# Optimization experiments

Hardware: AMD Instinct MI355X
Metric: run time of the kernel (lower is better)

## Reference

```python
import jax, jax.numpy as jnp
import numpy as np

D = 512
H = 8
LQ = 2048
LK = 8192
LARGE_NEG = 10000.0
CLAMP = 20.0


def setup_inputs() -> dict:
    key = jax.random.key(0)
    ks = jax.random.split(key, 9)
    Q = jax.random.normal(ks[0], (LQ, D), dtype=jnp.float32)
    K = jax.random.normal(ks[1], (LK, D), dtype=jnp.float32)
    V = jax.random.normal(ks[2], (LK, D), dtype=jnp.float32)
    key_padding_mask = jax.random.randint(ks[3], (LK,), 0, 2).astype(jnp.bool_)
    per_query_key_bias = jax.random.normal(ks[4], (LQ, LK), dtype=jnp.float32)
    # learned params of nn.MultiheadAttention: packed in_proj + out_proj
    s = 1.0 / np.sqrt(D)
    W_in = jax.random.uniform(ks[5], (3 * D, D), jnp.float32, -s, s)
    b_in = jnp.zeros((3 * D,), jnp.float32)
    W_out = jax.random.uniform(ks[6], (D, D), jnp.float32, -s, s)
    b_out = jnp.zeros((D,), jnp.float32)
    return {"Q": Q, "K": K, "V": V, "key_padding_mask": key_padding_mask,
            "per_query_key_bias": per_query_key_bias,
            "W_in": W_in, "b_in": b_in, "W_out": W_out, "b_out": b_out}


def reference(Q, K, V, key_padding_mask, per_query_key_bias, W_in, b_in, W_out, b_out):
    d = D // H
    # packed QKV projections (F.linear: x @ W.T + b)
    q = Q @ W_in[:D].T + b_in[:D]            # [Lq, D]
    k = K @ W_in[D:2 * D].T + b_in[D:2 * D]  # [Lk, D]
    v = V @ W_in[2 * D:].T + b_in[2 * D:]    # [Lk, D]
    q = q.reshape(LQ, H, d)
    k = k.reshape(LK, H, d)
    v = v.reshape(LK, H, d)
    scale = 1.0 / jnp.sqrt(jnp.asarray(d, q.dtype))
    scores = jnp.einsum('qhd,khd->hqk', q, k) * scale  # [H, Lq, Lk]
    scores = scores + per_query_key_bias[None, :, :]
    # column-only padding mask with large negative (no -inf)
    pad = key_padding_mask.astype(scores.dtype)[None, None, :]
    scores = scores - LARGE_NEG * pad
    # amax stabilization then clamp, then softmax
    scores = scores - jnp.max(scores, axis=-1, keepdims=True)
    scores = jnp.clip(scores, -CLAMP, CLAMP)
    attn = jax.nn.softmax(scores, axis=-1)
    out = jnp.einsum('hqk,khd->qhd', attn, v).reshape(LQ, D)
    out = out @ W_out.T + b_out
    return out
```

## Files before the change

### kernel.cpp

```cpp
#include <hip/hip_runtime.h>
#include <math.h>

#define DD 512
#define NH 8
#define HD 64
#define NLQ 2048
#define NLK 8192
#define LOG2E 1.4426950408889634f
#define SCQ (0.125f * LOG2E)

typedef __attribute__((ext_vector_type(8))) short bf16x8;
typedef __attribute__((ext_vector_type(8))) unsigned short u16x8;
typedef __attribute__((ext_vector_type(4))) float f32x4;

#define MFMA16(a, b, c) __builtin_amdgcn_mfma_f32_16x16x32_bf16((a), (b), (c), 0, 0, 0)

__device__ __forceinline__ unsigned short f2bf(float x) {
    unsigned u = __builtin_bit_cast(unsigned, x);
    u += 0x7fffu + ((u >> 16) & 1u);
    return (unsigned short)(u >> 16);
}
__device__ __forceinline__ float bf2f(unsigned short h) {
    unsigned u = ((unsigned)h) << 16;
    return __builtin_bit_cast(float, u);
}
__device__ __forceinline__ unsigned short f2h(float x) {
    return __builtin_bit_cast(unsigned short, (_Float16)x);
}
__device__ __forceinline__ float h2f(unsigned short u) {
    return (float)__builtin_bit_cast(_Float16, u);
}
__device__ __forceinline__ int cvtpk(float a, float b) {
    int r;
    asm("v_cvt_pk_bf16_f32 %0, %1, %2" : "=v"(r) : "v"(a), "v"(b));
    return r;
}
__device__ __forceinline__ float max3f(float a, float b, float c) {
    return fmaxf(fmaxf(a, b), c);
}
__device__ __forceinline__ float lobf(int w) {
    return __builtin_bit_cast(float, w << 16);
}
__device__ __forceinline__ float hibf(int w) {
    return __builtin_bit_cast(float, (int)(w & 0xffff0000));
}

#define NPROJ 576

__global__ __launch_bounds__(256) void prep(const float* __restrict__ Q,
                                            const float* __restrict__ K,
                                            const float* __restrict__ V,
                                            const float* __restrict__ Win,
                                            const float* __restrict__ bin,
                                            const float* __restrict__ bias,
                                            const int* __restrict__ mask,
                                            short* __restrict__ qhi,
                                            short* __restrict__ khi,
                                            short* __restrict__ vthi,
                                            unsigned short* __restrict__ bh)
{
    __shared__ __align__(16) short XsH[128 * 40];
    __shared__ __align__(16) short WsH[128 * 40];
    __shared__ __align__(16) short WsL[128 * 40];

    const int bid = blockIdx.x;
    if (bid >= NPROJ) {
        const int tid  = (bid - NPROJ) * 256 + threadIdx.x;
        const int tile = tid >> 6;
        const int l    = tid & 63;
        const int q    = (tile >> 7) * 16 + (l & 15);
        const int kb   = (tile & 127) * 64 + 4 * (l >> 4);
        u16x8 o0v, o1v;
#pragma unroll
        for (int j = 0; j < 4; ++j) {
            const float4 bv = *(const float4*)&bias[(size_t)q * NLK + kb + 16 * j];
            const int4   mv = *(const int4*)&mask[kb + 16 * j];
            const float a[4] = {bv.x, bv.y, bv.z, bv.w};
            const int   m[4] = {mv.x, mv.y, mv.z, mv.w};
#pragma unroll
            for (int r = 0; r < 4; ++r) {
                const float v = (a[r] - 10000.f * (float)m[r]) * LOG2E;
                const int idx = j * 4 + r;
                if (idx < 8) o0v[idx] = f2h(v);
                else         o1v[idx - 8] = f2h(v);
            }
        }
        const size_t base = ((size_t)tid) * 16;
        *(u16x8*)&bh[base] = o0v;
        *(u16x8*)&bh[base + 8] = o1v;
        return;
    }

    const int o0 = (bid / 144) * 128;
    const int bx = bid % 144;
    const float* X; const float* Wf; const float* b; short* out;
    int r0; float scale; int tr;
    if (bx < 16)      { X = Q; r0 = bx * 128;        Wf = Win;               b = bin;          out = qhi;  scale = SCQ; tr = 0; }
    else if (bx < 80) { X = K; r0 = (bx - 16) * 128; Wf = Win + DD * DD;     b = bin + DD;     out = khi;  scale = 1.f; tr = 0; }
    else              { X = V; r0 = (bx - 80) * 128; Wf = Win + 2 * DD * DD; b = bin + 2 * DD; out = vthi; scale = 1.f; tr = 1; }

    const int t    = threadIdx.x;
    const int wid  = t >> 6;
    const int lane = t & 63;
    const int g  = lane >> 4;
    const int c  = lane & 15;
    const int wr = wid >> 1;
    const int wc = wid & 1;
    const int srow = t >> 1;
    const int sk   = (t & 1) * 16;

    float4 xf[4], wf[4];
    auto ld = [&](int kc) {
#pragma unroll
        for (int i = 0; i < 4; ++i) {
            xf[i] = *(const float4*)&X[(size_t)(r0 + srow) * DD + kc + sk + 4 * i];
            wf[i] = *(const float4*)&Wf[(size_t)(o0 + srow) * DD + kc + sk + 4 * i];
        }
    };
    auto st = [&]() {
#pragma unroll
        for (int i = 0; i < 2; ++i) {
            int4 xw;
            xw.x = cvtpk(xf[2 * i].x, xf[2 * i].y);
            xw.y = cvtpk(xf[2 * i].z, xf[2 * i].w);
            xw.z = cvtpk(xf[2 * i + 1].x, xf[2 * i + 1].y);
            xw.w = cvtpk(xf[2 * i + 1].z, xf[2 * i + 1].w);
            *(int4*)&XsH[srow * 40 + sk + 8 * i] = xw;
            const float4 a = wf[2 * i], bb = wf[2 * i + 1];
            int4 hw;
            hw.x = cvtpk(a.x, a.y);
            hw.y = cvtpk(a.z, a.w);
            hw.z = cvtpk(bb.x, bb.y);
            hw.w = cvtpk(bb.z, bb.w);
            int4 lw;
            lw.x = cvtpk(a.x - lobf(hw.x), a.y - hibf(hw.x));
            lw.y = cvtpk(a.z - lobf(hw.y), a.w - hibf(hw.y));
            lw.z = cvtpk(bb.x - lobf(hw.z), bb.y - hibf(hw.z));
            lw.w = cvtpk(bb.z - lobf(hw.w), bb.w - hibf(hw.w));
            *(int4*)&WsH[srow * 40 + sk + 8 * i] = hw;
            *(int4*)&WsL[srow * 40 + sk + 8 * i] = lw;
        }
    };

    f32x4 acc[4][4];
#pragma unroll
    for (int i = 0; i < 4; ++i)
#pragma unroll
        for (int j = 0; j < 4; ++j) acc[i][j] = (f32x4){0.f, 0.f, 0.f, 0.f};

    ld(0);
    for (int kc = 0; kc < DD; kc += 32) {
        __syncthreads();
        st();
        __syncthreads();
        if (kc + 32 < DD) ld(kc + 32);

        bf16x8 ah[4], bhf[4], blf[4];
#pragma unroll
        for (int qg = 0; qg < 4; ++qg)
            ah[qg] = *(const bf16x8*)&XsH[(64 * wr + 16 * qg + c) * 40 + 8 * g];
#pragma unroll
        for (int og = 0; og < 4; ++og) {
            const int adr = (64 * wc + 16 * og + c) * 40 + 8 * g;
            bhf[og] = *(const bf16x8*)&WsH[adr];
            blf[og] = *(const bf16x8*)&WsL[adr];
        }
#pragma unroll
        for (int qg = 0; qg < 4; ++qg)
#pragma unroll
            for (int og = 0; og < 4; ++og) {
                acc[qg][og] = MFMA16(ah[qg], bhf[og], acc[qg][og]);
                acc[qg][og] = MFMA16(ah[qg], blf[og], acc[qg][og]);
            }
    }

#pragma unroll
    for (int qg = 0; qg < 4; ++qg)
#pragma unroll
        for (int og = 0; og < 4; ++og) {
            const int col = o0 + 64 * wc + 16 * og + c;
            const float bo = b[col];
#pragma unroll
            for (int r = 0; r < 4; ++r) {
                const int row = r0 + 64 * wr + 16 * qg + 4 * g + r;
                const float v = (acc[qg][og][r] + bo) * scale;
                if (tr) out[(size_t)col * NLK + row] = (short)f2bf(v);
                else    out[(size_t)row * DD + col]  = (short)f2bf(v);
            }
        }
}

__global__ __launch_bounds__(256) void gemm_out(const short* __restrict__ Xhi,
                                                const short* __restrict__ Xlo,
                                                const float* __restrict__ Wf,
                                                const float* __restrict__ b,
                                                float* __restrict__ Y)
{
    __shared__ __align__(16) short XsH[64 * 40];
    __shared__ __align__(16) short XsL[64 * 40];
    __shared__ __align__(16) short WsH[64 * 40];
    __shared__ __align__(16) short WsL[64 * 40];

    const int r0 = blockIdx.x * 64;
    const int o0 = blockIdx.y * 64;
    const int t    = threadIdx.x;
    const int wid  = t >> 6;
    const int lane = t & 63;
    const int g  = lane >> 4;
    const int c  = lane & 15;
    const int srow = t >> 2;
    const int sc8  = (t & 3) * 8;

    bf16x8 pxh, pxl;
    float4 wf0, wf1;
    auto ld = [&](int kc) {
        pxh = *(const bf16x8*)&Xhi[(size_t)(r0 + srow) * DD + kc + sc8];
        pxl = *(const bf16x8*)&Xlo[(size_t)(r0 + srow) * DD + kc + sc8];
        wf0 = *(const float4*)&Wf[(size_t)(o0 + srow) * DD + kc + sc8];
        wf1 = *(const float4*)&Wf[(size_t)(o0 + srow) * DD + kc + sc8 + 4];
    };
    auto st = [&]() {
        *(bf16x8*)&XsH[srow * 40 + sc8] = pxh;
        *(bf16x8*)&XsL[srow * 40 + sc8] = pxl;
        int4 hw;
        hw.x = cvtpk(wf0.x, wf0.y);
        hw.y = cvtpk(wf0.z, wf0.w);
        hw.z = cvtpk(wf1.x, wf1.y);
        hw.w = cvtpk(wf1.z, wf1.w);
        int4 lw;
        lw.x = cvtpk(wf0.x - lobf(hw.x), wf0.y - hibf(hw.x));
        lw.y = cvtpk(wf0.z - lobf(hw.y), wf0.w - hibf(hw.y));
        lw.z = cvtpk(wf1.x - lobf(hw.z), wf1.y - hibf(hw.z));
        lw.w = cvtpk(wf1.z - lobf(hw.w), wf1.w - hibf(hw.w));
        *(int4*)&WsH[srow * 40 + sc8] = hw;
        *(int4*)&WsL[srow * 40 + sc8] = lw;
    };

    f32x4 acc[4];
#pragma unroll
    for (int n = 0; n < 4; ++n) acc[n] = (f32x4){0.f, 0.f, 0.f, 0.f};

    ld(0);
    for (int kc = 0; kc < DD; kc += 32) {
        __syncthreads();
        st();
        __syncthreads();
        if (kc + 32 < DD) ld(kc + 32);

        bf16x8 ah, al, bh[4], bl[4];
        ah = *(const bf16x8*)&XsH[(wid * 16 + c) * 40 + 8 * g];
        al = *(const bf16x8*)&XsL[(wid * 16 + c) * 40 + 8 * g];
#pragma unroll
        for (int n = 0; n < 4; ++n) {
            const int adr = (16 * n + c) * 40 + 8 * g;
            bh[n] = *(const bf16x8*)&WsH[adr];
            bl[n] = *(const bf16x8*)&WsL[adr];
        }
#pragma unroll
        for (int n = 0; n < 4; ++n) {
            acc[n] = MFMA16(ah, bh[n], acc[n]);
            acc[n] = MFMA16(ah, bl[n], acc[n]);
            acc[n] = MFMA16(al, bh[n], acc[n]);
        }
    }

#pragma unroll
    for (int n = 0; n < 4; ++n) {
        const int col = o0 + 16 * n + c;
        const float bo = b[col];
#pragma unroll
        for (int r = 0; r < 4; ++r)
            Y[(size_t)(r0 + wid * 16 + 4 * g + r) * DD + col] = acc[n][r] + bo;
    }
}

#define QT 128
#define KT 64
#define NKC 8
#define CHUNK (NLK / NKC)
#define NT (CHUNK / KT)

__global__ __launch_bounds__(512, 4) void attn_mfma(const short* __restrict__ qhi,
                                                    const short* __restrict__ khi,
                                                    const short* __restrict__ vthi,
                                                    const unsigned short* __restrict__ biash,
                                                    unsigned short* __restrict__ macc,
                                                    float2* __restrict__ mlb)
{
    __shared__ __align__(16) short ksh[2 * KT * HD];
    __shared__ __align__(16) short vth[2 * KT * HD];
    __shared__ __align__(16) short psh[8 * 16 * KT];

    const int id = blockIdx.x;
    const int h  = id >> 7;
    const int qt = (id >> 3) & 15;
    const int kc = id & 7;
    const int q0 = qt * QT;
    const int k0 = kc * CHUNK;

    const int t    = threadIdx.x;
    const int wid  = t >> 6;
    const int lane = t & 63;
    const int g  = lane >> 4;
    const int cl = lane & 15;
    const int swc = ((cl & 7) << 3);

    bf16x8 qah[2];
    {
        const size_t qr = (size_t)(q0 + wid * 16 + cl) * DD + h * HD;
        qah[0] = *(const bf16x8*)&qhi[qr + 8 * g];
        qah[1] = *(const bf16x8*)&qhi[qr + 32 + 8 * g];
    }

    const int v0 = (8 * g) ^ swc;
    const short* kbA0 = &ksh[cl * HD + v0];
    const short* kbB0 = &ksh[cl * HD + (v0 ^ 32)];
    const short* kbA1 = kbA0 + KT * HD;
    const short* kbB1 = kbB0 + KT * HD;
    const short* vbA0 = &vth[cl * HD + v0];
    const short* vbB0 = &vth[cl * HD + (v0 ^ 32)];
    const short* vbA1 = vbA0 + KT * HD;
    const short* vbB1 = vbB0 + KT * HD;

    const int kr0 = t >> 3;
    const int db0 = (t & 7) * 8;
    const int sw0 = ((kr0 & 7) << 3);
    short* wk0 = &ksh[kr0 * HD + (db0 ^ sw0)];
    short* wk1 = wk0 + KT * HD;
    short* wv0 = &vth[kr0 * HD + (db0 ^ sw0)];
    short* wv1 = wv0 + KT * HD;

    short* psw = &psh[wid * (16 * KT)];
    short* pw0 = &psw[cl * KT + (( 0 + 4 * g) ^ swc)];
    short* pw1 = &psw[cl * KT + ((16 + 4 * g) ^ swc)];
    short* pw2 = &psw[cl * KT + ((32 + 4 * g) ^ swc)];
    short* pw3 = &psw[cl * KT + ((48 + 4 * g) ^ swc)];
    const short* pr0 = &psw[cl * KT + ((8 * g) ^ swc)];
    const short* pr1 = &psw[cl * KT + ((32 + 8 * g) ^ swc)];

    const short* kgp = khi + (size_t)(k0 + kr0) * DD + h * HD + db0;
    const short* vgp = vthi + (size_t)(h * HD + kr0) * NLK + k0 + db0;
    const unsigned short* bgp =
        biash + (((size_t)(qt * 8 + wid) * 128 + kc * NT) << 10) + lane * 16;

    bf16x8 rkh, rvh;
    u16x8 bp0, bp1;
    rkh = *(const bf16x8*)kgp;  kgp += (size_t)KT * DD;
    rvh = *(const bf16x8*)vgp;  vgp += KT;
    bp0 = *(const u16x8*)bgp;
    bp1 = *(const u16x8*)(bgp + 8);  bgp += 1024;

    bf16x8 ones;
#pragma unroll
    for (int i = 0; i < 8; ++i) ones[i] = (short)0x3F80;

    f32x4 acco[4];
    f32x4 lacc = (f32x4){0.f, 0.f, 0.f, 0.f};
#pragma unroll
    for (int n = 0; n < 4; ++n) acco[n] = (f32x4){0.f, 0.f, 0.f, 0.f};
    float m_ = -1e30f;

    for (int it = 0; it < NT; ++it) {
        const int p = it & 1;
        const short* kA = p ? kbA1 : kbA0;
        const short* kB = p ? kbB1 : kbB0;
        const short* vA = p ? vbA1 : vbA0;
        const short* vB = p ? vbB1 : vbB0;
        short* wk = p ? wk1 : wk0;
        short* wv = p ? wv1 : wv0;

        *(bf16x8*)wk = rkh;
        *(bf16x8*)wv = rvh;
        __syncthreads();
        if (it + 1 < NT) {
            rkh = *(const bf16x8*)kgp;  kgp += (size_t)KT * DD;
            rvh = *(const bf16x8*)vgp;  vgp += KT;
        }

        f32x4 sc[4];
#pragma unroll
        for (int j = 0; j < 4; ++j)
#pragma unroll
            for (int r = 0; r < 4; ++r) {
                const int i = j * 4 + r;
                sc[j][r] = h2f((i < 8) ? (unsigned short)bp0[i]
                                       : (unsigned short)bp1[i - 8]);
            }

        __builtin_amdgcn_s_setprio(1);
#pragma unroll
        for (int j = 0; j < 4; ++j) {
            const bf16x8 kf0 = *(const bf16x8*)(kA + j * 16 * HD);
            const bf16x8 kf1 = *(const bf16x8*)(kB + j * 16 * HD);
            sc[j] = MFMA16(kf0, qah[0], sc[j]);
            sc[j] = MFMA16(kf1, qah[1], sc[j]);
        }
        __builtin_amdgcn_s_setprio(0);

        if (it + 1 < NT) {
            bp0 = *(const u16x8*)bgp;
            bp1 = *(const u16x8*)(bgp + 8);  bgp += 1024;
        }

        const float t0 = max3f(sc[0][0], sc[0][1], sc[0][2]);
        const float t1 = max3f(sc[0][3], sc[1][0], sc[1][1]);
        const float t2 = max3f(sc[1][2], sc[1][3], sc[2][0]);
        const float t3 = max3f(sc[2][1], sc[2][2], sc[2][3]);
        const float t4 = max3f(sc[3][0], sc[3][1], sc[3][2]);
        float tm = max3f(max3f(t0, t1, t2), max3f(t3, t4, sc[3][3]),
                         -1e30f);
        tm = fmaxf(tm, __shfl_xor(tm, 16));
        tm = fmaxf(tm, __shfl_xor(tm, 32));
        if (!__all(tm - m_ <= 11.5f)) {
            const float mn = fmaxf(m_, tm);
            const float al = exp2f(m_ - mn);
            float alr[4];
#pragma unroll
            for (int r = 0; r < 4; ++r) alr[r] = __shfl(al, 4 * g + r);
#pragma unroll
            for (int n = 0; n < 4; ++n)
#pragma unroll
                for (int r = 0; r < 4; ++r) acco[n][r] *= alr[r];
#pragma unroll
            for (int r = 0; r < 4; ++r) lacc[r] *= alr[r];
            m_ = mn;
        }
#pragma unroll
        for (int j = 0; j < 4; ++j)
#pragma unroll
            for (int r = 0; r < 4; ++r)
                sc[j][r] = exp2f(sc[j][r] - m_);

        *(int2*)pw0 = make_int2(cvtpk(sc[0][0], sc[0][1]), cvtpk(sc[0][2], sc[0][3]));
        *(int2*)pw1 = make_int2(cvtpk(sc[1][0], sc[1][1]), cvtpk(sc[1][2], sc[1][3]));
        *(int2*)pw2 = make_int2(cvtpk(sc[2][0], sc[2][1]), cvtpk(sc[2][2], sc[2][3]));
        *(int2*)pw3 = make_int2(cvtpk(sc[3][0], sc[3][1]), cvtpk(sc[3][2], sc[3][3]));
        bf16x8 pah[2];
        pah[0] = *(const bf16x8*)pr0;
        pah[1] = *(const bf16x8*)pr1;

        __builtin_amdgcn_s_setprio(1);
#pragma unroll
        for (int n = 0; n < 4; ++n) {
            const bf16x8 vh0 = *(const bf16x8*)(vA + n * 16 * HD);
            const bf16x8 vh1 = *(const bf16x8*)(vB + n * 16 * HD);
            acco[n] = MFMA16(pah[0], vh0, acco[n]);
            acco[n] = MFMA16(pah[1], vh1, acco[n]);
        }
        lacc = MFMA16(pah[0], ones, lacc);
        lacc = MFMA16(pah[1], ones, lacc);
        __builtin_amdgcn_s_setprio(0);
    }

    f32x4 linv;
#pragma unroll
    for (int r = 0; r < 4; ++r) linv[r] = 1.f / lacc[r];
#pragma unroll
    for (int r = 0; r < 4; ++r) {
        const int q = q0 + wid * 16 + 4 * g + r;
        const size_t base = ((size_t)(kc * NH + h) * NLQ + q) * HD;
#pragma unroll
        for (int n = 0; n < 4; ++n)
            macc[base + 16 * n + cl] = f2h(acco[n][r] * linv[r]);
    }
    {
        const int srcl = ((cl >> 2) << 4) + cl;
        const float lc0 = __shfl(lacc[0], srcl);
        const float lc1 = __shfl(lacc[1], srcl);
        const float lc2 = __shfl(lacc[2], srcl);
        const float lc3 = __shfl(lacc[3], srcl);
        const int rr = cl & 3;
        const float lq = rr == 0 ? lc0 : rr == 1 ? lc1 : rr == 2 ? lc2 : lc3;
        if (g == 0)
            mlb[(size_t)(kc * NH + h) * NLQ + q0 + wid * 16 + cl] = make_float2(m_, lq);
    }
}

__global__ __launch_bounds__(256) void attn_combine(const unsigned short* __restrict__ macc,
                                                    const float2* __restrict__ mlb,
                                                    short* __restrict__ aohi,
                                                    short* __restrict__ aolo)
{
    const int row = blockIdx.x * 4 + (threadIdx.x >> 6);
    const int d   = threadIdx.x & 63;
    float m[NKC], l[NKC];
#pragma unroll
    for (int c = 0; c < NKC; ++c) {
        const float2 v = mlb[(size_t)c * NH * NLQ + row];
        m[c] = v.x; l[c] = v.y;
    }
    float M = m[0];
#pragma unroll
    for (int c = 1; c < NKC; ++c) M = fmaxf(M, m[c]);
    float w[NKC], L = 0.f;
#pragma unroll
    for (int c = 0; c < NKC; ++c) { w[c] = exp2f(m[c] - M) * l[c]; L += w[c]; }
    float s = 0.f;
#pragma unroll
    for (int c = 0; c < NKC; ++c)
        s += h2f(macc[((size_t)c * NH * NLQ + row) * HD + d]) * w[c];
    const float v = s / L;
    const int hh = row >> 11;
    const int q  = row & (NLQ - 1);
    const size_t o = (size_t)q * DD + hh * HD + d;
    const unsigned short hb = f2bf(v);
    aohi[o] = (short)hb;
    aolo[o] = (short)f2bf(v - bf2f(hb));
}

extern "C" void kernel_launch(void* const* d_in, const int* in_sizes, int n_in,
                              void* d_out, int out_size, void* d_ws, size_t ws_size,
                              hipStream_t stream)
{
    (void)in_sizes; (void)n_in; (void)out_size; (void)ws_size;
    const float* Q    = (const float*)d_in[0];
    const float* K    = (const float*)d_in[1];
    const float* V    = (const float*)d_in[2];
    const int*   mask = (const int*)d_in[3];
    const float* bias = (const float*)d_in[4];
    const float* Win  = (const float*)d_in[5];
    const float* bin  = (const float*)d_in[6];
    const float* Wout = (const float*)d_in[7];
    const float* bout = (const float*)d_in[8];
    float* out = (float*)d_out;

    short* qhi_  = (short*)d_ws;
    short* khi_  = qhi_  + (size_t)NLQ * DD;
    short* vthi_ = khi_  + (size_t)NLK * DD;
    unsigned short* biash_ = (unsigned short*)(vthi_ + (size_t)NLK * DD);
    unsigned short* macc_  = biash_ + (size_t)NLQ * NLK;
    float2* ml_  = (float2*)(macc_ + (size_t)NKC * NH * NLQ * HD);
    short* aohi_ = (short*)(ml_ + (size_t)NKC * NH * NLQ);
    short* aolo_ = aohi_ + (size_t)NLQ * DD;

    prep<<<dim3(NPROJ + 4096), 256, 0, stream>>>(Q, K, V, Win, bin, bias, mask,
                                                 qhi_, khi_, vthi_, biash_);

    attn_mfma<<<dim3(NH * 16 * NKC), 512, 0, stream>>>(qhi_, khi_, vthi_, biash_, macc_, ml_);

    attn_combine<<<dim3(NH * NLQ / 4), 256, 0, stream>>>(macc_, ml_, aohi_, aolo_);

    gemm_out<<<dim3(NLQ / 64, DD / 64), 256, 0, stream>>>(aohi_, aolo_, Wout, bout, out);
}
```

Baseline: 145.1 us.

## Process two 16-row query subtiles per wave to double K/V reuse

```diff
diff --git a/kernel.cpp b/kernel.cpp
--- a/kernel.cpp
+++ b/kernel.cpp
@@ -274,11 +274,12 @@
     }
 }
 
-#define QT 128
+#define QT 256
 #define KT 64
 #define NKC 8
 #define CHUNK (NLK / NKC)
 #define NT (CHUNK / KT)
+#define BOFF (128 * 1024)
 
 __global__ __launch_bounds__(512, 4) void attn_mfma(const short* __restrict__ qhi,
                                                     const short* __restrict__ khi,
@@ -292,8 +293,8 @@
     __shared__ __align__(16) short psh[8 * 16 * KT];
 
     const int id = blockIdx.x;
-    const int h  = id >> 7;
-    const int qt = (id >> 3) & 15;
+    const int h  = id >> 6;
+    const int qt = (id >> 3) & 7;
     const int kc = id & 7;
     const int q0 = qt * QT;
     const int k0 = kc * CHUNK;
@@ -305,11 +306,13 @@
     const int cl = lane & 15;
     const int swc = ((cl & 7) << 3);
 
-    bf16x8 qah[2];
+    bf16x8 qaA[2], qaB[2];
     {
-        const size_t qr = (size_t)(q0 + wid * 16 + cl) * DD + h * HD;
-        qah[0] = *(const bf16x8*)&qhi[qr + 8 * g];
-        qah[1] = *(const bf16x8*)&qhi[qr + 32 + 8 * g];
+        const size_t qrA = (size_t)(q0 + wid * 32 + cl) * DD + h * HD;
+        qaA[0] = *(const bf16x8*)&qhi[qrA + 8 * g];
+        qaA[1] = *(const bf16x8*)&qhi[qrA + 32 + 8 * g];
+        qaB[0] = *(const bf16x8*)&qhi[qrA + 16 * DD + 8 * g];
+        qaB[1] = *(const bf16x8*)&qhi[qrA + 16 * DD + 32 + 8 * g];
     }
 
     const int v0 = (8 * g) ^ swc;
@@ -341,24 +344,68 @@
     const short* kgp = khi + (size_t)(k0 + kr0) * DD + h * HD + db0;
     const short* vgp = vthi + (size_t)(h * HD + kr0) * NLK + k0 + db0;
     const unsigned short* bgp =
-        biash + (((size_t)(qt * 8 + wid) * 128 + kc * NT) << 10) + lane * 16;
+        biash + (((size_t)(qt * 16 + wid * 2) * 128 + kc * NT) << 10) + lane * 16;
 
     bf16x8 rkh, rvh;
-    u16x8 bp0, bp1;
+    u16x8 bpA0, bpA1, bpB0, bpB1;
     rkh = *(const bf16x8*)kgp;  kgp += (size_t)KT * DD;
     rvh = *(const bf16x8*)vgp;  vgp += KT;
-    bp0 = *(const u16x8*)bgp;
-    bp1 = *(const u16x8*)(bgp + 8);  bgp += 1024;
+    bpA0 = *(const u16x8*)bgp;
+    bpA1 = *(const u16x8*)(bgp + 8);
+    bpB0 = *(const u16x8*)(bgp + BOFF);
+    bpB1 = *(const u16x8*)(bgp + BOFF + 8);
+    bgp += 1024;
 
     bf16x8 ones;
 #pragma unroll
     for (int i = 0; i < 8; ++i) ones[i] = (short)0x3F80;
 
-    f32x4 acco[4];
-    f32x4 lacc = (f32x4){0.f, 0.f, 0.f, 0.f};
-#pragma unroll
-    for (int n = 0; n < 4; ++n) acco[n] = (f32x4){0.f, 0.f, 0.f, 0.f};
-    float m_ = -1e30f;
+    f32x4 accA[4], accB[4];
+    f32x4 lacA = (f32x4){0.f, 0.f, 0.f, 0.f};
+    f32x4 lacB = (f32x4){0.f, 0.f, 0.f, 0.f};
+#pragma unroll
+    for (int n = 0; n < 4; ++n) {
+        accA[n] = (f32x4){0.f, 0.f, 0.f, 0.f};
+        accB[n] = (f32x4){0.f, 0.f, 0.f, 0.f};
+    }
+    float mA = -1e30f, mB = -1e30f;
+
+    auto softmax_pack = [&](f32x4 (&sc)[4], f32x4 (&acc)[4], f32x4 &lac,
+                            float &mm, bf16x8 (&pa)[2]) {
+        const float t0 = max3f(sc[0][0], sc[0][1], sc[0][2]);
+        const float t1 = max3f(sc[0][3], sc[1][0], sc[1][1]);
+        const float t2 = max3f(sc[1][2], sc[1][3], sc[2][0]);
+        const float t3 = max3f(sc[2][1], sc[2][2], sc[2][3]);
+        const float t4 = max3f(sc[3][0], sc[3][1], sc[3][2]);
+        float tm = max3f(max3f(t0, t1, t2), max3f(t3, t4, sc[3][3]), -1e30f);
+        tm = fmaxf(tm, __shfl_xor(tm, 16));
+        tm = fmaxf(tm, __shfl_xor(tm, 32));
+        if (!__all(tm - mm <= 11.5f)) {
+            const float mn = fmaxf(mm, tm);
+            const float al = exp2f(mm - mn);
+            float alr[4];
+#pragma unroll
+            for (int r = 0; r < 4; ++r) alr[r] = __shfl(al, 4 * g + r);
+#pragma unroll
+            for (int n = 0; n < 4; ++n)
+#pragma unroll
+                for (int r = 0; r < 4; ++r) acc[n][r] *= alr[r];
+#pragma unroll
+            for (int r = 0; r < 4; ++r) lac[r] *= alr[r];
+            mm = mn;
+        }
+#pragma unroll
+        for (int j = 0; j < 4; ++j)
+#pragma unroll
+            for (int r = 0; r < 4; ++r)
+                sc[j][r] = exp2f(sc[j][r] - mm);
+        *(int2*)pw0 = make_int2(cvtpk(sc[0][0], sc[0][1]), cvtpk(sc[0][2], sc[0][3]));
+        *(int2*)pw1 = make_int2(cvtpk(sc[1][0], sc[1][1]), cvtpk(sc[1][2], sc[1][3]));
+        *(int2*)pw2 = make_int2(cvtpk(sc[2][0], sc[2][1]), cvtpk(sc[2][2], sc[2][3]));
+        *(int2*)pw3 = make_int2(cvtpk(sc[3][0], sc[3][1]), cvtpk(sc[3][2], sc[3][3]));
+        pa[0] = *(const bf16x8*)pr0;
+        pa[1] = *(const bf16x8*)pr1;
+    };
 
     for (int it = 0; it < NT; ++it) {
         const int p = it & 1;
@@ -377,14 +424,16 @@
             rvh = *(const bf16x8*)vgp;  vgp += KT;
         }
 
-        f32x4 sc[4];
+        f32x4 scA[4], scB[4];
 #pragma unroll
         for (int j = 0; j < 4; ++j)
 #pragma unroll
             for (int r = 0; r < 4; ++r) {
                 const int i = j * 4 + r;
-                sc[j][r] = h2f((i < 8) ? (unsigned short)bp0[i]
-                                       : (unsigned short)bp1[i - 8]);
+                scA[j][r] = h2f((i < 8) ? (unsigned short)bpA0[i]
+                                        : (unsigned short)bpA1[i - 8]);
+                scB[j][r] = h2f((i < 8) ? (unsigned short)bpB0[i]
+                                        : (unsigned short)bpB1[i - 8]);
             }
 
         __builtin_amdgcn_s_setprio(1);
@@ -392,88 +441,66 @@
         for (int j = 0; j < 4; ++j) {
             const bf16x8 kf0 = *(const bf16x8*)(kA + j * 16 * HD);
             const bf16x8 kf1 = *(const bf16x8*)(kB + j * 16 * HD);
-            sc[j] = MFMA16(kf0, qah[0], sc[j]);
-            sc[j] = MFMA16(kf1, qah[1], sc[j]);
+            scA[j] = MFMA16(kf0, qaA[0], scA[j]);
+            scA[j] = MFMA16(kf1, qaA[1], scA[j]);
+            scB[j] = MFMA16(kf0, qaB[0], scB[j]);
+            scB[j] = MFMA16(kf1, qaB[1], scB[j]);
         }
         __builtin_amdgcn_s_setprio(0);
 
-        if (it + 1 < NT) {
-            bp0 = *(const u16x8*)bgp;
-            bp1 = *(const u16x8*)(bgp + 8);  bgp += 1024;
-        }
-
-        const float t0 = max3f(sc[0][0], sc[0][1], sc[0][2]);
-        const float t1 = max3f(sc[0][3], sc[1][0], sc[1][1]);
-        const float t2 = max3f(sc[1][2], sc[1][3], sc[2][0]);
-        const float t3 = max3f(sc[2][1], sc[2][2], sc[2][3]);
-        const float t4 = max3f(sc[3][0], sc[3][1], sc[3][2]);
-        float tm = max3f(max3f(t0, t1, t2), max3f(t3, t4, sc[3][3]),
-                         -1e30f);
-        tm = fmaxf(tm, __shfl_xor(tm, 16));
-        tm = fmaxf(tm, __shfl_xor(tm, 32));
-        if (!__all(tm - m_ <= 11.5f)) {
-            const float mn = fmaxf(m_, tm);
-            const float al = exp2f(m_ - mn);
-            float alr[4];
-#pragma unroll
-            for (int r = 0; r < 4; ++r) alr[r] = __shfl(al, 4 * g + r);
-#pragma unroll
-            for (int n = 0; n < 4; ++n)
-#pragma unroll
-                for (int r = 0; r < 4; ++r) acco[n][r] *= alr[r];
-#pragma unroll
-            for (int r = 0; r < 4; ++r) lacc[r] *= alr[r];
-            m_ = mn;
-        }
-#pragma unroll
-        for (int j = 0; j < 4; ++j)
-#pragma unroll
-            for (int r = 0; r < 4; ++r)
-                sc[j][r] = exp2f(sc[j][r] - m_);
-
-        *(int2*)pw0 = make_int2(cvtpk(sc[0][0], sc[0][1]), cvtpk(sc[0][2], sc[0][3]));
-        *(int2*)pw1 = make_int2(cvtpk(sc[1][0], sc[1][1]), cvtpk(sc[1][2], sc[1][3]));
-        *(int2*)pw2 = make_int2(cvtpk(sc[2][0], sc[2][1]), cvtpk(sc[2][2], sc[2][3]));
-        *(int2*)pw3 = make_int2(cvtpk(sc[3][0], sc[3][1]), cvtpk(sc[3][2], sc[3][3]));
-        bf16x8 pah[2];
-        pah[0] = *(const bf16x8*)pr0;
-        pah[1] = *(const bf16x8*)pr1;
+        bf16x8 paA[2], paB[2];
+        softmax_pack(scA, accA, lacA, mA, paA);
+        softmax_pack(scB, accB, lacB, mB, paB);
 
         __builtin_amdgcn_s_setprio(1);
 #pragma unroll
         for (int n = 0; n < 4; ++n) {
             const bf16x8 vh0 = *(const bf16x8*)(vA + n * 16 * HD);
             const bf16x8 vh1 = *(const bf16x8*)(vB + n * 16 * HD);
-            acco[n] = MFMA16(pah[0], vh0, acco[n]);
-            acco[n] = MFMA16(pah[1], vh1, acco[n]);
-        }
-        lacc = MFMA16(pah[0], ones, lacc);
-        lacc = MFMA16(pah[1], ones, lacc);
+            accA[n] = MFMA16(paA[0], vh0, accA[n]);
+            accA[n] = MFMA16(paA[1], vh1, accA[n]);
+            accB[n] = MFMA16(paB[0], vh0, accB[n]);
+            accB[n] = MFMA16(paB[1], vh1, accB[n]);
+        }
+        lacA = MFMA16(paA[0], ones, lacA);
+        lacA = MFMA16(paA[1], ones, lacA);
+        lacB = MFMA16(paB[0], ones, lacB);
+        lacB = MFMA16(paB[1], ones, lacB);
         __builtin_amdgcn_s_setprio(0);
-    }
-
-    f32x4 linv;
-#pragma unroll
-    for (int r = 0; r < 4; ++r) linv[r] = 1.f / lacc[r];
-#pragma unroll
-    for (int r = 0; r < 4; ++r) {
-        const int q = q0 + wid * 16 + 4 * g + r;
-        const size_t base = ((size_t)(kc * NH + h) * NLQ + q) * HD;
-#pragma unroll
-        for (int n = 0; n < 4; ++n)
-            macc[base + 16 * n + cl] = f2h(acco[n][r] * linv[r]);
-    }
-    {
+
+        if (it + 1 < NT) {
+            bpA0 = *(const u16x8*)bgp;
+            bpA1 = *(const u16x8*)(bgp + 8);
+            bpB0 = *(const u16x8*)(bgp + BOFF);
+            bpB1 = *(const u16x8*)(bgp + BOFF + 8);
+            bgp += 1024;
+        }
+    }
+
+    auto epilogue = [&](f32x4 (&acc)[4], f32x4 &lac, float mm, int qbase) {
+        f32x4 linv;
+#pragma unroll
+        for (int r = 0; r < 4; ++r) linv[r] = 1.f / lac[r];
+#pragma unroll
+        for (int r = 0; r < 4; ++r) {
+            const int q = qbase + 4 * g + r;
+            const size_t base = ((size_t)(kc * NH + h) * NLQ + q) * HD;
+#pragma unroll
+            for (int n = 0; n < 4; ++n)
+                macc[base + 16 * n + cl] = f2h(acc[n][r] * linv[r]);
+        }
         const int srcl = ((cl >> 2) << 4) + cl;
-        const float lc0 = __shfl(lacc[0], srcl);
-        const float lc1 = __shfl(lacc[1], srcl);
-        const float lc2 = __shfl(lacc[2], srcl);
-        const float lc3 = __shfl(lacc[3], srcl);
+        const float lc0 = __shfl(lac[0], srcl);
+        const float lc1 = __shfl(lac[1], srcl);
+        const float lc2 = __shfl(lac[2], srcl);
+        const float lc3 = __shfl(lac[3], srcl);
         const int rr = cl & 3;
         const float lq = rr == 0 ? lc0 : rr == 1 ? lc1 : rr == 2 ? lc2 : lc3;
         if (g == 0)
-            mlb[(size_t)(kc * NH + h) * NLQ + q0 + wid * 16 + cl] = make_float2(m_, lq);
-    }
+            mlb[(size_t)(kc * NH + h) * NLQ + qbase + cl] = make_float2(mm, lq);
+    };
+    epilogue(accA, lacA, mA, q0 + wid * 32);
+    epilogue(accB, lacB, mB, q0 + wid * 32 + 16);
 }
 
 __global__ __launch_bounds__(256) void attn_combine(const unsigned short* __restrict__ macc,
@@ -536,7 +563,7 @@
     prep<<<dim3(NPROJ + 4096), 256, 0, stream>>>(Q, K, V, Win, bin, bias, mask,
                                                  qhi_, khi_, vthi_, biash_);
 
-    attn_mfma<<<dim3(NH * 16 * NKC), 512, 0, stream>>>(qhi_, khi_, vthi_, biash_, macc_, ml_);
+    attn_mfma<<<dim3(NH * 8 * NKC), 512, 0, stream>>>(qhi_, khi_, vthi_, biash_, macc_, ml_);
 
     attn_combine<<<dim3(NH * NLQ / 4), 256, 0, stream>>>(macc_, ml_, aohi_, aolo_);
 
```

New measurement: 149.0 us. 1.03x slower.
